# Optimization experiments

Hardware: AMD Instinct MI355X
Metric: run time of the kernel (lower is better)

## Reference

```python
import jax, jax.numpy as jnp
import numpy as np

B, T, D, K = 8, 2048, 384, 64

def setup_inputs() -> dict:
    key = jax.random.key(0)
    k1, k2, k3, k4 = jax.random.split(key, 4)
    x = jax.random.normal(k1, (B, T, D), dtype=jnp.float32)
    # torch nn.Linear default init scale ~ 1/sqrt(fan_in); use scaled normals
    Wq = jax.random.normal(k2, (D, K), dtype=jnp.float32) / np.sqrt(D)
    Wk = jax.random.normal(k3, (D, K), dtype=jnp.float32) / np.sqrt(D)
    Wv = jax.random.normal(k4, (D, D), dtype=jnp.float32) / np.sqrt(D)
    return {"x": x, "Wq": Wq, "Wk": Wk, "Wv": Wv}

def reference(x, Wq, Wk, Wv):
    # x: (B,T,D)
    q = jnp.einsum('btd,dk->btk', x, Wq)      # (B,T,K)
    k = jnp.einsum('btd,dk->btk', x, Wk)      # (B,T,K)
    v = jnp.einsum('btd,de->bte', x, Wv)      # (B,T,D)
    scores = jnp.einsum('bqk,bsk->bqs', q, k) / jnp.sqrt(jnp.float32(K))  # (B,T,T)
    causal = jnp.tril(jnp.ones((T, T), dtype=bool))
    scores = jnp.where(causal, scores, -jnp.inf)
    weights = jax.nn.softmax(scores, axis=-1)
    out = jnp.einsum('bqs,bse->bqe', weights, v)  # (B,T,D)
    return out
```

## Files before the change

### kernel.cpp

```cpp
#include <hip/hip_runtime.h>

#define TT 2048
#define DD 384

typedef float f32x4 __attribute__((ext_vector_type(4)));
typedef float f32x16 __attribute__((ext_vector_type(16)));
typedef short s16x8 __attribute__((ext_vector_type(8)));
typedef short s16x2 __attribute__((ext_vector_type(2)));
typedef unsigned int u32x4 __attribute__((ext_vector_type(4)));

typedef __attribute__((address_space(3))) unsigned char* as3p;
typedef const __attribute__((address_space(1))) unsigned char* as1p;
#define GLLDS(gsrc, ldst) __builtin_amdgcn_global_load_lds((as1p)(gsrc), (as3p)(ldst), 16, 0, 0)

static __device__ __forceinline__ unsigned short f2bf(float f) {
    unsigned int u = __builtin_bit_cast(unsigned int, f);
    u = (u + 0x7fffu + ((u >> 16) & 1u)) >> 16;
    return (unsigned short)u;
}
static __device__ __forceinline__ unsigned int pk2(float a, float b) {
#if __has_builtin(__builtin_amdgcn_cvt_pk_bf16_f32)
    s16x2 t = __builtin_amdgcn_cvt_pk_bf16_f32(a, b);
    return __builtin_bit_cast(unsigned int, t);
#else
    unsigned int ua = __builtin_bit_cast(unsigned int, a);
    unsigned int ub = __builtin_bit_cast(unsigned int, b);
    ua = (ua + 0x7fffu + ((ua >> 16) & 1u)) >> 16;
    ub = (ub + 0x7fffu + ((ub >> 16) & 1u)) & 0xffff0000u;
    return ua | ub;
#endif
}

__global__ __launch_bounds__(256, 2) void qkv_gemm(
    const float* __restrict__ x, const float* __restrict__ Wq,
    const float* __restrict__ Wk, const float* __restrict__ Wv,
    unsigned short* __restrict__ qo, unsigned short* __restrict__ ko,
    unsigned short* __restrict__ vto)
{
    __shared__ __align__(16) unsigned short lds[16384];
    const int tid = threadIdx.x;
    const int l   = tid & 63;
    const int w   = tid >> 6;
    const int si  = l & 15;
    const int qq  = l >> 4;
    const int m0  = blockIdx.x * 128;
    const int nb  = blockIdx.y;
    const int wr  = w >> 1, wc = w & 1;

    const int bn = tid & 127;
    const int bk = (tid >> 7) * 16;
    const float* wsrc; int ldw;
    if (nb == 0) { wsrc = (bn < 64) ? (Wq + bn) : (Wk + (bn - 64)); ldw = 64; }
    else         { wsrc = Wv + (nb - 1) * 128 + bn;                 ldw = 384; }

    f32x4 acc[4][4];
    #pragma unroll
    for (int rt = 0; rt < 4; ++rt)
        #pragma unroll
        for (int ct = 0; ct < 4; ++ct) acc[rt][ct] = (f32x4){0.f, 0.f, 0.f, 0.f};

    for (int kt = 0; kt < 12; ++kt) {
        const int k0 = kt * 32;
        #pragma unroll
        for (int i = 0; i < 2; ++i) {
            const int u = tid + 256 * i, r = u >> 2, c = u & 3;
            const float* xp = x + (size_t)(m0 + r) * DD + k0 + c * 8;
            f32x4 x0 = *(const f32x4*)xp;
            f32x4 x1 = *(const f32x4*)(xp + 4);
            s16x8 av;
            av[0] = (short)f2bf(x0[0]); av[1] = (short)f2bf(x0[1]);
            av[2] = (short)f2bf(x0[2]); av[3] = (short)f2bf(x0[3]);
            av[4] = (short)f2bf(x1[0]); av[5] = (short)f2bf(x1[1]);
            av[6] = (short)f2bf(x1[2]); av[7] = (short)f2bf(x1[3]);
            *(s16x8*)&lds[r * 32 + ((c ^ (r & 3)) * 8)] = av;
        }
        {
            float t[16];
            #pragma unroll
            for (int j = 0; j < 16; ++j) t[j] = wsrc[(size_t)(k0 + bk + j) * ldw];
            #pragma unroll
            for (int jj = 0; jj < 2; ++jj) {
                s16x8 bv;
                #pragma unroll
                for (int j = 0; j < 8; ++j) bv[j] = (short)f2bf(t[jj * 8 + j]);
                const int ch = (tid >> 7) * 2 + jj;
                *(s16x8*)&lds[4096 + bn * 32 + ((ch ^ (bn & 3)) * 8)] = bv;
            }
        }
        __syncthreads();

        s16x8 af[4], bf[4];
        #pragma unroll
        for (int rt = 0; rt < 4; ++rt) {
            const int row = wr * 64 + rt * 16 + si;
            af[rt] = *(const s16x8*)&lds[row * 32 + ((qq ^ (row & 3)) * 8)];
        }
        #pragma unroll
        for (int ct = 0; ct < 4; ++ct) {
            const int col = wc * 64 + ct * 16 + si;
            bf[ct] = *(const s16x8*)&lds[4096 + col * 32 + ((qq ^ (col & 3)) * 8)];
        }
        #pragma unroll
        for (int rt = 0; rt < 4; ++rt)
            #pragma unroll
            for (int ct = 0; ct < 4; ++ct)
                acc[rt][ct] = __builtin_amdgcn_mfma_f32_16x16x32_bf16(af[rt], bf[ct], acc[rt][ct], 0, 0, 0);
        __syncthreads();
    }

    if (nb == 0) {
        if (wc == 0) {
            #pragma unroll
            for (int rt = 0; rt < 4; ++rt)
                #pragma unroll
                for (int ct = 0; ct < 4; ++ct)
                    #pragma unroll
                    for (int r = 0; r < 4; ++r) {
                        const int m = m0 + wr * 64 + rt * 16 + qq * 4 + r;
                        qo[(size_t)m * 64 + ct * 16 + si] = f2bf(acc[rt][ct][r] * 0.125f);
                    }
        } else {
            #pragma unroll
            for (int rt = 0; rt < 4; ++rt)
                #pragma unroll
                for (int ct = 0; ct < 4; ++ct)
                    #pragma unroll
                    for (int r = 0; r < 4; ++r) {
                        const int m = m0 + wr * 64 + rt * 16 + qq * 4 + r;
                        const int col = ct * 16 + si;
                        ko[(size_t)m * 64 + (((col >> 3) ^ (m & 7)) * 8) + (col & 7)] = f2bf(acc[rt][ct][r]);
                    }
        }
    } else {
        #pragma unroll
        for (int rt = 0; rt < 4; ++rt)
            #pragma unroll
            for (int ct = 0; ct < 4; ++ct)
                #pragma unroll
                for (int r = 0; r < 4; ++r) {
                    const int m = wr * 64 + rt * 16 + qq * 4 + r;
                    const int n = wc * 64 + ct * 16 + si;
                    lds[n * 128 + (((m >> 3) ^ (n & 7)) * 8) + (m & 7)] = f2bf(acc[rt][ct][r]);
                }
        __syncthreads();
        const int bbat = m0 >> 11, t0 = m0 & 2047;
        #pragma unroll
        for (int i = 0; i < 8; ++i) {
            const int u = tid + 256 * i, n = u >> 4, mc = u & 15;
            s16x8 v = *(const s16x8*)&lds[n * 128 + ((mc ^ (n & 7)) * 8)];
            *(s16x8*)&vto[((size_t)bbat * DD + ((nb - 1) * 128 + n)) * TT
                          + t0 + (mc >> 3) * 64 + (((mc & 7) ^ (n & 7)) * 8)] = v;
        }
    }
}

__global__ __launch_bounds__(256, 2) void attn(
    const unsigned short* __restrict__ qg, const unsigned short* __restrict__ kg,
    const unsigned short* __restrict__ vg, float* __restrict__ out)
{
    __shared__ __align__(16) unsigned short lds[40960];

    const int tid = threadIdx.x;
    const int l   = tid & 63;
    const int w   = tid >> 6;
    const int qh  = w >> 1;
    const int eg  = w & 1;
    const int lo  = l & 31;
    const int hi  = l >> 5;

    const int g    = blockIdx.x;
    const int bb   = g & 7;
    const int rest = g >> 3;
    const int eh   = rest % 3;
    const int q2   = 31 - rest / 3;
    const int q0   = q2 * 64;
    const int e0   = eh * 128;
    const int qrow = q0 + qh * 32 + lo;

    s16x8 qf[4];
    {
        const unsigned short* qp = qg + ((size_t)bb * TT + qrow) * 64;
        #pragma unroll
        for (int st = 0; st < 4; ++st) qf[st] = *(const s16x8*)(qp + st * 16 + hi * 8);
    }

    f32x16 o[2];
    #pragma unroll
    for (int et = 0; et < 2; ++et)
        #pragma unroll
        for (int r = 0; r < 16; ++r) o[et][r] = 0.f;
    float lp = 0.f;

    const unsigned short* kbase = kg + (size_t)bb * TT * 64;
    const unsigned short* vbase = vg + ((size_t)bb * DD + e0) * TT;

    #define STAGE(IT, KB, VB)                                                              \
    {                                                                                      \
        GLLDS(kbase + (size_t)(IT) * 4096 + (2 * w) * 512 + l * 8,                         \
              &lds[(KB) * 4096 + (2 * w) * 512]);                                          \
        GLLDS(kbase + (size_t)(IT) * 4096 + (2 * w + 1) * 512 + l * 8,                     \
              &lds[(KB) * 4096 + (2 * w + 1) * 512]);                                      \
        _Pragma("unroll")                                                                  \
        for (int c3 = 0; c3 < 4; ++c3) {                                                   \
            const int rg = 4 * w + c3;                                                     \
            GLLDS(vbase + (size_t)(rg * 8 + (l >> 3)) * TT + (IT) * 64 + (l & 7) * 8,      \
                  &lds[8192 + (VB) * 8192 + rg * 512]);                                    \
        }                                                                                  \
    }

    #define PVSTEP(VB, PB)                                                                 \
    {                                                                                      \
        _Pragma("unroll")                                                                  \
        for (int ss = 0; ss < 2; ++ss) {                                                   \
            s16x8 a0 = *(const s16x8*)&lds[32768 + (PB) * 4096 + (qh * 2 + ss) * 1024 + l * 8];       \
            s16x8 a1 = *(const s16x8*)&lds[32768 + (PB) * 4096 + (qh * 2 + ss) * 1024 + 512 + l * 8]; \
            _Pragma("unroll")                                                              \
            for (int et = 0; et < 2; ++et) {                                               \
                const int el = eg * 64 + et * 32 + lo;                                     \
                const int vbse = 8192 + (VB) * 8192 + el * 64;                             \
                s16x8 v0 = *(const s16x8*)&lds[vbse + (((ss * 4 + hi) ^ (el & 7)) * 8)];   \
                o[et] = __builtin_amdgcn_mfma_f32_32x32x16_bf16(a0, v0, o[et], 0, 0, 0);   \
                s16x8 v1 = *(const s16x8*)&lds[vbse + (((ss * 4 + 2 + hi) ^ (el & 7)) * 8)]; \
                o[et] = __builtin_amdgcn_mfma_f32_32x32x16_bf16(a1, v1, o[et], 0, 0, 0);   \
            }                                                                              \
        }                                                                                  \
    }

    STAGE(0, 0, 0);

    int vi = 0, vn = 1;
    for (int it = 0; it <= q2; ++it) {
        const int kb = it & 1;
        __syncthreads();

        if (it < q2) STAGE(it + 1, 1 - kb, vn);

        {
            f32x16 sa;
            #pragma unroll
            for (int r = 0; r < 16; ++r) sa[r] = 0.f;
            #pragma unroll
            for (int st = 0; st < 4; ++st) {
                s16x8 kf = *(const s16x8*)&lds[kb * 4096 + (eg * 32 + lo) * 64 + (((st * 2 + hi) ^ (lo & 7)) * 8)];
                sa = __builtin_amdgcn_mfma_f32_32x32x16_bf16(kf, qf[st], sa, 0, 0, 0);
            }
            const bool mb = (it == q2);
            float pv[16];
            #pragma unroll
            for (int r = 0; r < 16; ++r) {
                float e = __expf(sa[r]);
                if (mb) {
                    const int srow = it * 64 + eg * 32 + (r & 3) + 8 * (r >> 2) + 4 * hi;
                    if (srow > qrow) e = 0.f;
                }
                pv[r] = e;
                lp += e;
            }
            unsigned int d0 = pk2(pv[0], pv[1]),   d1 = pk2(pv[2], pv[3]);
            unsigned int d2 = pk2(pv[4], pv[5]),   d3 = pk2(pv[6], pv[7]);
            unsigned int d4 = pk2(pv[8], pv[9]),   d5 = pk2(pv[10], pv[11]);
            unsigned int d6 = pk2(pv[12], pv[13]), d7 = pk2(pv[14], pv[15]);
            unsigned int sA0 = hi ? d0 : d2, sA1 = hi ? d1 : d3;
            unsigned int rA0 = (unsigned int)__shfl_xor((int)sA0, 32);
            unsigned int rA1 = (unsigned int)__shfl_xor((int)sA1, 32);
            u32x4 fa0 = hi ? (u32x4){rA0, rA1, d2, d3} : (u32x4){d0, d1, rA0, rA1};
            unsigned int sB0 = hi ? d4 : d6, sB1 = hi ? d5 : d7;
            unsigned int rB0 = (unsigned int)__shfl_xor((int)sB0, 32);
            unsigned int rB1 = (unsigned int)__shfl_xor((int)sB1, 32);
            u32x4 fa1 = hi ? (u32x4){rB0, rB1, d6, d7} : (u32x4){d4, d5, rB0, rB1};
            *(s16x8*)&lds[32768 + kb * 4096 + (qh * 2 + eg) * 1024 + l * 8]       = __builtin_bit_cast(s16x8, fa0);
            *(s16x8*)&lds[32768 + kb * 4096 + (qh * 2 + eg) * 1024 + 512 + l * 8] = __builtin_bit_cast(s16x8, fa1);
        }

        if (it > 0) {
            const int vp = (vi == 0) ? 2 : vi - 1;
            PVSTEP(vp, 1 - kb);
        }

        vi = vn; vn = (vn == 2) ? 0 : vn + 1;
    }
    __syncthreads();
    {
        const int vlast = (vi == 0) ? 2 : vi - 1;
        PVSTEP(vlast, q2 & 1);
    }
    __syncthreads();

    float* stL = (float*)&lds[32768];
    lp += __shfl_xor(lp, 32);
    if (hi == 0) stL[(qh * 2 + eg) * 32 + lo] = lp;
    __syncthreads();

    #pragma unroll
    for (int et = 0; et < 2; ++et)
        #pragma unroll
        for (int r = 0; r < 16; ++r) {
            const int rloc = (r & 3) + 8 * (r >> 2) + 4 * hi;
            const float linv = 1.f / (stL[qh * 64 + rloc] + stL[qh * 64 + 32 + rloc]);
            out[((size_t)bb * TT + q0 + qh * 32 + rloc) * DD + e0 + eg * 64 + et * 32 + lo]
                = o[et][r] * linv;
        }
    #undef STAGE
    #undef PVSTEP
}

extern "C" void kernel_launch(void* const* d_in, const int* in_sizes, int n_in,
                              void* d_out, int out_size, void* d_ws, size_t ws_size,
                              hipStream_t stream)
{
    const float* x  = (const float*)d_in[0];
    const float* Wq = (const float*)d_in[1];
    const float* Wk = (const float*)d_in[2];
    const float* Wv = (const float*)d_in[3];

    unsigned short* qws  = (unsigned short*)d_ws;
    unsigned short* kws  = (unsigned short*)((char*)d_ws + ((size_t)2 << 20));
    unsigned short* vtws = (unsigned short*)((char*)d_ws + ((size_t)4 << 20));

    qkv_gemm<<<dim3(128, 4), dim3(256), 0, stream>>>(x, Wq, Wk, Wv, qws, kws, vtws);
    attn<<<dim3(768), dim3(256), 0, stream>>>(qws, kws, vtws, (float*)d_out);
}
```

Before: 140.3 us.

## Pre-convert inputs to bf16, double-buffer QKV GEMM, warp-specialize attention

A new pre-pass kernel converts x and the concatenated weights to swizzled bf16 buffers in workspace. The QKV GEMM then streams them with direct global-to-LDS loads into double-buffered LDS, replacing the in-loop fp32 loads and conversions. The attention kernel is split into producer waves, which compute QK^T and softmax numerators for both query halves, and consumer waves, which run the PV MFMAs, so the two phases overlap. The extra launch and the bf16 round trip through global memory add traffic, and the consumer waves hold twice as many accumulators, raising register pressure.

```diff
diff --git a/kernel.cpp b/kernel.cpp
--- a/kernel.cpp
+++ b/kernel.cpp
@@ -31,9 +31,51 @@
 #endif
 }
 
-__global__ __launch_bounds__(256, 2) void qkv_gemm(
+__global__ __launch_bounds__(256, 8) void xwprep(
     const float* __restrict__ x, const float* __restrict__ Wq,
     const float* __restrict__ Wk, const float* __restrict__ Wv,
+    unsigned short* __restrict__ xbf, unsigned short* __restrict__ wall)
+{
+    const int gid = blockIdx.x * 256 + threadIdx.x;
+    if (gid < 196608) {
+        const int kt = gid >> 14;
+        const int m  = gid & 16383;
+        const float* xp = x + (size_t)m * 384 + kt * 32;
+        unsigned short* op = xbf + (size_t)m * 384 + kt * 32;
+        #pragma unroll
+        for (int c = 0; c < 4; ++c) {
+            f32x4 a = *(const f32x4*)(xp + c * 8);
+            f32x4 b = *(const f32x4*)(xp + c * 8 + 4);
+            s16x8 v;
+            v[0] = (short)f2bf(a[0]); v[1] = (short)f2bf(a[1]);
+            v[2] = (short)f2bf(a[2]); v[3] = (short)f2bf(a[3]);
+            v[4] = (short)f2bf(b[0]); v[5] = (short)f2bf(b[1]);
+            v[6] = (short)f2bf(b[2]); v[7] = (short)f2bf(b[3]);
+            *(s16x8*)(op + ((c ^ (m & 3)) * 8)) = v;
+        }
+    } else {
+        const int gid2 = gid - 196608;
+        const int col = gid2 & 511;
+        const int kt  = gid2 >> 9;
+        unsigned short* op = wall + (size_t)col * 384 + kt * 32;
+        #pragma unroll
+        for (int c = 0; c < 4; ++c) {
+            s16x8 v;
+            #pragma unroll
+            for (int k7 = 0; k7 < 8; ++k7) {
+                const int k = kt * 32 + c * 8 + k7;
+                float f = (col < 64)  ? Wq[(size_t)k * 64 + col]
+                        : (col < 128) ? Wk[(size_t)k * 64 + (col - 64)]
+                                      : Wv[(size_t)k * 384 + (col - 128)];
+                v[k7] = (short)f2bf(f);
+            }
+            *(s16x8*)(op + ((c ^ (col & 3)) * 8)) = v;
+        }
+    }
+}
+
+__global__ __launch_bounds__(256, 4) void qkv_gemm(
+    const unsigned short* __restrict__ xbf, const unsigned short* __restrict__ wall,
     unsigned short* __restrict__ qo, unsigned short* __restrict__ ko,
     unsigned short* __restrict__ vto)
 {
@@ -47,11 +89,18 @@
     const int nb  = blockIdx.y;
     const int wr  = w >> 1, wc = w & 1;
 
-    const int bn = tid & 127;
-    const int bk = (tid >> 7) * 16;
-    const float* wsrc; int ldw;
-    if (nb == 0) { wsrc = (bn < 64) ? (Wq + bn) : (Wk + (bn - 64)); ldw = 64; }
-    else         { wsrc = Wv + (nb - 1) * 128 + bn;                 ldw = 384; }
+    const unsigned short* asrc = xbf + ((size_t)m0 + (l >> 2)) * 384 + (l & 3) * 8;
+    const unsigned short* bsrc = wall + ((size_t)(nb * 128) + (l >> 2)) * 384 + (l & 3) * 8;
+
+#define QSTAGE(KT, B)                                                                     \
+    {                                                                                     \
+        _Pragma("unroll")                                                                 \
+        for (int i = 0; i < 2; ++i) {                                                     \
+            const int u = w * 2 + i;                                                      \
+            GLLDS(asrc + (size_t)(u * 16) * 384 + (KT) * 32, &lds[(B) * 8192 + u * 512]); \
+            GLLDS(bsrc + (size_t)(u * 16) * 384 + (KT) * 32, &lds[(B) * 8192 + 4096 + u * 512]); \
+        }                                                                                 \
+    }
 
     f32x4 acc[4][4];
     #pragma unroll
@@ -59,54 +108,31 @@
         #pragma unroll
         for (int ct = 0; ct < 4; ++ct) acc[rt][ct] = (f32x4){0.f, 0.f, 0.f, 0.f};
 
+    QSTAGE(0, 0);
     for (int kt = 0; kt < 12; ++kt) {
-        const int k0 = kt * 32;
-        #pragma unroll
-        for (int i = 0; i < 2; ++i) {
-            const int u = tid + 256 * i, r = u >> 2, c = u & 3;
-            const float* xp = x + (size_t)(m0 + r) * DD + k0 + c * 8;
-            f32x4 x0 = *(const f32x4*)xp;
-            f32x4 x1 = *(const f32x4*)(xp + 4);
-            s16x8 av;
-            av[0] = (short)f2bf(x0[0]); av[1] = (short)f2bf(x0[1]);
-            av[2] = (short)f2bf(x0[2]); av[3] = (short)f2bf(x0[3]);
-            av[4] = (short)f2bf(x1[0]); av[5] = (short)f2bf(x1[1]);
-            av[6] = (short)f2bf(x1[2]); av[7] = (short)f2bf(x1[3]);
-            *(s16x8*)&lds[r * 32 + ((c ^ (r & 3)) * 8)] = av;
-        }
-        {
-            float t[16];
-            #pragma unroll
-            for (int j = 0; j < 16; ++j) t[j] = wsrc[(size_t)(k0 + bk + j) * ldw];
-            #pragma unroll
-            for (int jj = 0; jj < 2; ++jj) {
-                s16x8 bv;
-                #pragma unroll
-                for (int j = 0; j < 8; ++j) bv[j] = (short)f2bf(t[jj * 8 + j]);
-                const int ch = (tid >> 7) * 2 + jj;
-                *(s16x8*)&lds[4096 + bn * 32 + ((ch ^ (bn & 3)) * 8)] = bv;
-            }
-        }
+        const int b = kt & 1;
         __syncthreads();
+        if (kt < 11) QSTAGE(kt + 1, 1 - b);
 
         s16x8 af[4], bf[4];
         #pragma unroll
         for (int rt = 0; rt < 4; ++rt) {
             const int row = wr * 64 + rt * 16 + si;
-            af[rt] = *(const s16x8*)&lds[row * 32 + ((qq ^ (row & 3)) * 8)];
+            af[rt] = *(const s16x8*)&lds[b * 8192 + row * 32 + ((qq ^ (row & 3)) * 8)];
         }
         #pragma unroll
         for (int ct = 0; ct < 4; ++ct) {
             const int col = wc * 64 + ct * 16 + si;
-            bf[ct] = *(const s16x8*)&lds[4096 + col * 32 + ((qq ^ (col & 3)) * 8)];
+            bf[ct] = *(const s16x8*)&lds[b * 8192 + 4096 + col * 32 + ((qq ^ (col & 3)) * 8)];
         }
         #pragma unroll
         for (int rt = 0; rt < 4; ++rt)
             #pragma unroll
             for (int ct = 0; ct < 4; ++ct)
                 acc[rt][ct] = __builtin_amdgcn_mfma_f32_16x16x32_bf16(af[rt], bf[ct], acc[rt][ct], 0, 0, 0);
-        __syncthreads();
-    }
+    }
+    __syncthreads();
+#undef QSTAGE
 
     if (nb == 0) {
         if (wc == 0) {
@@ -163,8 +189,8 @@
     const int tid = threadIdx.x;
     const int l   = tid & 63;
     const int w   = tid >> 6;
-    const int qh  = w >> 1;
-    const int eg  = w & 1;
+    const int ri  = w & 1;
+    const int prod = (w < 2);
     const int lo  = l & 31;
     const int hi  = l >> 5;
 
@@ -175,53 +201,67 @@
     const int q2   = 31 - rest / 3;
     const int q0   = q2 * 64;
     const int e0   = eh * 128;
-    const int qrow = q0 + qh * 32 + lo;
-
-    s16x8 qf[4];
-    {
-        const unsigned short* qp = qg + ((size_t)bb * TT + qrow) * 64;
-        #pragma unroll
-        for (int st = 0; st < 4; ++st) qf[st] = *(const s16x8*)(qp + st * 16 + hi * 8);
-    }
-
-    f32x16 o[2];
+
+    s16x8 qf2[2][4];
+    if (prod) {
+        #pragma unroll
+        for (int qh = 0; qh < 2; ++qh) {
+            const unsigned short* qp = qg + ((size_t)bb * TT + q0 + qh * 32 + lo) * 64;
+            #pragma unroll
+            for (int st = 0; st < 4; ++st) qf2[qh][st] = *(const s16x8*)(qp + st * 16 + hi * 8);
+        }
+    }
+
+    f32x16 o4[2][2];
     #pragma unroll
-    for (int et = 0; et < 2; ++et)
-        #pragma unroll
-        for (int r = 0; r < 16; ++r) o[et][r] = 0.f;
-    float lp = 0.f;
+    for (int qh = 0; qh < 2; ++qh)
+        #pragma unroll
+        for (int et = 0; et < 2; ++et)
+            #pragma unroll
+            for (int r = 0; r < 16; ++r) o4[qh][et][r] = 0.f;
+    float lp2[2] = {0.f, 0.f};
 
     const unsigned short* kbase = kg + (size_t)bb * TT * 64;
     const unsigned short* vbase = vg + ((size_t)bb * DD + e0) * TT;
 
-    #define STAGE(IT, KB, VB)                                                              \
+#define STAGE(IT, KB, VB)                                                                  \
     {                                                                                      \
-        GLLDS(kbase + (size_t)(IT) * 4096 + (2 * w) * 512 + l * 8,                         \
-              &lds[(KB) * 4096 + (2 * w) * 512]);                                          \
-        GLLDS(kbase + (size_t)(IT) * 4096 + (2 * w + 1) * 512 + l * 8,                     \
-              &lds[(KB) * 4096 + (2 * w + 1) * 512]);                                      \
-        _Pragma("unroll")                                                                  \
-        for (int c3 = 0; c3 < 4; ++c3) {                                                   \
-            const int rg = 4 * w + c3;                                                     \
-            GLLDS(vbase + (size_t)(rg * 8 + (l >> 3)) * TT + (IT) * 64 + (l & 7) * 8,      \
-                  &lds[8192 + (VB) * 8192 + rg * 512]);                                    \
+        if (prod) {                                                                        \
+            _Pragma("unroll")                                                              \
+            for (int c4 = 0; c4 < 4; ++c4) {                                               \
+                const int ch = w * 4 + c4;                                                 \
+                GLLDS(kbase + (size_t)(IT) * 4096 + ch * 512 + l * 8,                      \
+                      &lds[(KB) * 4096 + ch * 512]);                                       \
+            }                                                                              \
+        } else {                                                                           \
+            _Pragma("unroll")                                                              \
+            for (int c8 = 0; c8 < 8; ++c8) {                                               \
+                const int rg = ri * 8 + c8;                                                \
+                GLLDS(vbase + (size_t)(rg * 8 + (l >> 3)) * TT + (IT) * 64 + (l & 7) * 8,  \
+                      &lds[8192 + (VB) * 8192 + rg * 512]);                                \
+            }                                                                              \
         }                                                                                  \
     }
 
-    #define PVSTEP(VB, PB)                                                                 \
+#define PVC(VB, PB)                                                                        \
     {                                                                                      \
         _Pragma("unroll")                                                                  \
-        for (int ss = 0; ss < 2; ++ss) {                                                   \
-            s16x8 a0 = *(const s16x8*)&lds[32768 + (PB) * 4096 + (qh * 2 + ss) * 1024 + l * 8];       \
-            s16x8 a1 = *(const s16x8*)&lds[32768 + (PB) * 4096 + (qh * 2 + ss) * 1024 + 512 + l * 8]; \
+        for (int s2 = 0; s2 < 2; ++s2) {                                                   \
+            const int pbse = 32768 + (PB) * 4096 + s2 * 1024;                              \
+            s16x8 a00 = *(const s16x8*)&lds[pbse + l * 8];                                 \
+            s16x8 a01 = *(const s16x8*)&lds[pbse + 512 + l * 8];                           \
+            s16x8 a10 = *(const s16x8*)&lds[pbse + 2048 + l * 8];                          \
+            s16x8 a11 = *(const s16x8*)&lds[pbse + 2560 + l * 8];                          \
             _Pragma("unroll")                                                              \
             for (int et = 0; et < 2; ++et) {                                               \
-                const int el = eg * 64 + et * 32 + lo;                                     \
+                const int el = ri * 64 + et * 32 + lo;                                     \
                 const int vbse = 8192 + (VB) * 8192 + el * 64;                             \
-                s16x8 v0 = *(const s16x8*)&lds[vbse + (((ss * 4 + hi) ^ (el & 7)) * 8)];   \
-                o[et] = __builtin_amdgcn_mfma_f32_32x32x16_bf16(a0, v0, o[et], 0, 0, 0);   \
-                s16x8 v1 = *(const s16x8*)&lds[vbse + (((ss * 4 + 2 + hi) ^ (el & 7)) * 8)]; \
-                o[et] = __builtin_amdgcn_mfma_f32_32x32x16_bf16(a1, v1, o[et], 0, 0, 0);   \
+                s16x8 v0 = *(const s16x8*)&lds[vbse + (((s2 * 4 + hi) ^ (el & 7)) * 8)];   \
+                s16x8 v1 = *(const s16x8*)&lds[vbse + (((s2 * 4 + 2 + hi) ^ (el & 7)) * 8)]; \
+                o4[0][et] = __builtin_amdgcn_mfma_f32_32x32x16_bf16(a00, v0, o4[0][et], 0, 0, 0); \
+                o4[0][et] = __builtin_amdgcn_mfma_f32_32x32x16_bf16(a01, v1, o4[0][et], 0, 0, 0); \
+                o4[1][et] = __builtin_amdgcn_mfma_f32_32x32x16_bf16(a10, v0, o4[1][et], 0, 0, 0); \
+                o4[1][et] = __builtin_amdgcn_mfma_f32_32x32x16_bf16(a11, v1, o4[1][et], 0, 0, 0); \
             }                                                                              \
         }                                                                                  \
     }
@@ -235,73 +275,84 @@
 
         if (it < q2) STAGE(it + 1, 1 - kb, vn);
 
-        {
-            f32x16 sa;
-            #pragma unroll
-            for (int r = 0; r < 16; ++r) sa[r] = 0.f;
-            #pragma unroll
-            for (int st = 0; st < 4; ++st) {
-                s16x8 kf = *(const s16x8*)&lds[kb * 4096 + (eg * 32 + lo) * 64 + (((st * 2 + hi) ^ (lo & 7)) * 8)];
-                sa = __builtin_amdgcn_mfma_f32_32x32x16_bf16(kf, qf[st], sa, 0, 0, 0);
+        if (prod) {
+            const bool mb = (it == q2);
+            s16x8 kfr[4];
+            #pragma unroll
+            for (int st = 0; st < 4; ++st)
+                kfr[st] = *(const s16x8*)&lds[kb * 4096 + (ri * 32 + lo) * 64 + (((st * 2 + hi) ^ (lo & 7)) * 8)];
+            #pragma unroll
+            for (int qh = 0; qh < 2; ++qh) {
+                const int qrow = q0 + qh * 32 + lo;
+                f32x16 sa;
+                #pragma unroll
+                for (int r = 0; r < 16; ++r) sa[r] = 0.f;
+                #pragma unroll
+                for (int st = 0; st < 4; ++st)
+                    sa = __builtin_amdgcn_mfma_f32_32x32x16_bf16(kfr[st], qf2[qh][st], sa, 0, 0, 0);
+                float pv[16];
+                #pragma unroll
+                for (int r = 0; r < 16; ++r) {
+                    float e = __expf(sa[r]);
+                    if (mb) {
+                        const int srow = it * 64 + ri * 32 + (r & 3) + 8 * (r >> 2) + 4 * hi;
+                        if (srow > qrow) e = 0.f;
+                    }
+                    pv[r] = e;
+                    lp2[qh] += e;
+                }
+                unsigned int d0 = pk2(pv[0], pv[1]),   d1 = pk2(pv[2], pv[3]);
+                unsigned int d2 = pk2(pv[4], pv[5]),   d3 = pk2(pv[6], pv[7]);
+                unsigned int d4 = pk2(pv[8], pv[9]),   d5 = pk2(pv[10], pv[11]);
+                unsigned int d6 = pk2(pv[12], pv[13]), d7 = pk2(pv[14], pv[15]);
+                unsigned int sA0 = hi ? d0 : d2, sA1 = hi ? d1 : d3;
+                unsigned int rA0 = (unsigned int)__shfl_xor((int)sA0, 32);
+                unsigned int rA1 = (unsigned int)__shfl_xor((int)sA1, 32);
+                u32x4 fa0 = hi ? (u32x4){rA0, rA1, d2, d3} : (u32x4){d0, d1, rA0, rA1};
+                unsigned int sB0 = hi ? d4 : d6, sB1 = hi ? d5 : d7;
+                unsigned int rB0 = (unsigned int)__shfl_xor((int)sB0, 32);
+                unsigned int rB1 = (unsigned int)__shfl_xor((int)sB1, 32);
+                u32x4 fa1 = hi ? (u32x4){rB0, rB1, d6, d7} : (u32x4){d4, d5, rB0, rB1};
+                *(s16x8*)&lds[32768 + kb * 4096 + (qh * 2 + ri) * 1024 + l * 8]       = __builtin_bit_cast(s16x8, fa0);
+                *(s16x8*)&lds[32768 + kb * 4096 + (qh * 2 + ri) * 1024 + 512 + l * 8] = __builtin_bit_cast(s16x8, fa1);
             }
-            const bool mb = (it == q2);
-            float pv[16];
-            #pragma unroll
-            for (int r = 0; r < 16; ++r) {
-                float e = __expf(sa[r]);
-                if (mb) {
-                    const int srow = it * 64 + eg * 32 + (r & 3) + 8 * (r >> 2) + 4 * hi;
-                    if (srow > qrow) e = 0.f;
+        } else if (it > 0) {
+            const int vp = (vi == 0) ? 2 : vi - 1;
+            PVC(vp, 1 - kb);
+        }
+
+        vi = vn; vn = (vn == 2) ? 0 : vn + 1;
+    }
+    __syncthreads();
+
+    if (prod) {
+        #pragma unroll
+        for (int qh = 0; qh < 2; ++qh) {
+            float lp = lp2[qh] + __shfl_xor(lp2[qh], 32);
+            if (hi == 0) ((float*)lds)[(qh * 2 + ri) * 32 + lo] = lp;
+        }
+    } else {
+        const int vlast = (vi == 0) ? 2 : vi - 1;
+        PVC(vlast, q2 & 1);
+    }
+    __syncthreads();
+
+    if (!prod) {
+        const float* stL = (const float*)lds;
+        #pragma unroll
+        for (int qh = 0; qh < 2; ++qh)
+            #pragma unroll
+            for (int et = 0; et < 2; ++et)
+                #pragma unroll
+                for (int r = 0; r < 16; ++r) {
+                    const int rloc = (r & 3) + 8 * (r >> 2) + 4 * hi;
+                    const float linv = 1.f / (stL[qh * 64 + rloc] + stL[qh * 64 + 32 + rloc]);
+                    out[((size_t)bb * TT + q0 + qh * 32 + rloc) * DD + e0 + ri * 64 + et * 32 + lo]
+                        = o4[qh][et][r] * linv;
                 }
-                pv[r] = e;
-                lp += e;
-            }
-            unsigned int d0 = pk2(pv[0], pv[1]),   d1 = pk2(pv[2], pv[3]);
-            unsigned int d2 = pk2(pv[4], pv[5]),   d3 = pk2(pv[6], pv[7]);
-            unsigned int d4 = pk2(pv[8], pv[9]),   d5 = pk2(pv[10], pv[11]);
-            unsigned int d6 = pk2(pv[12], pv[13]), d7 = pk2(pv[14], pv[15]);
-            unsigned int sA0 = hi ? d0 : d2, sA1 = hi ? d1 : d3;
-            unsigned int rA0 = (unsigned int)__shfl_xor((int)sA0, 32);
-            unsigned int rA1 = (unsigned int)__shfl_xor((int)sA1, 32);
-            u32x4 fa0 = hi ? (u32x4){rA0, rA1, d2, d3} : (u32x4){d0, d1, rA0, rA1};
-            unsigned int sB0 = hi ? d4 : d6, sB1 = hi ? d5 : d7;
-            unsigned int rB0 = (unsigned int)__shfl_xor((int)sB0, 32);
-            unsigned int rB1 = (unsigned int)__shfl_xor((int)sB1, 32);
-            u32x4 fa1 = hi ? (u32x4){rB0, rB1, d6, d7} : (u32x4){d4, d5, rB0, rB1};
-            *(s16x8*)&lds[32768 + kb * 4096 + (qh * 2 + eg) * 1024 + l * 8]       = __builtin_bit_cast(s16x8, fa0);
-            *(s16x8*)&lds[32768 + kb * 4096 + (qh * 2 + eg) * 1024 + 512 + l * 8] = __builtin_bit_cast(s16x8, fa1);
-        }
-
-        if (it > 0) {
-            const int vp = (vi == 0) ? 2 : vi - 1;
-            PVSTEP(vp, 1 - kb);
-        }
-
-        vi = vn; vn = (vn == 2) ? 0 : vn + 1;
-    }
-    __syncthreads();
-    {
-        const int vlast = (vi == 0) ? 2 : vi - 1;
-        PVSTEP(vlast, q2 & 1);
-    }
-    __syncthreads();
-
-    float* stL = (float*)&lds[32768];
-    lp += __shfl_xor(lp, 32);
-    if (hi == 0) stL[(qh * 2 + eg) * 32 + lo] = lp;
-    __syncthreads();
-
-    #pragma unroll
-    for (int et = 0; et < 2; ++et)
-        #pragma unroll
-        for (int r = 0; r < 16; ++r) {
-            const int rloc = (r & 3) + 8 * (r >> 2) + 4 * hi;
-            const float linv = 1.f / (stL[qh * 64 + rloc] + stL[qh * 64 + 32 + rloc]);
-            out[((size_t)bb * TT + q0 + qh * 32 + rloc) * DD + e0 + eg * 64 + et * 32 + lo]
-                = o[et][r] * linv;
-        }
-    #undef STAGE
-    #undef PVSTEP
+    }
+#undef STAGE
+#undef PVC
 }
 
 extern "C" void kernel_launch(void* const* d_in, const int* in_sizes, int n_in,
@@ -316,7 +367,10 @@
     unsigned short* qws  = (unsigned short*)d_ws;
     unsigned short* kws  = (unsigned short*)((char*)d_ws + ((size_t)2 << 20));
     unsigned short* vtws = (unsigned short*)((char*)d_ws + ((size_t)4 << 20));
-
-    qkv_gemm<<<dim3(128, 4), dim3(256), 0, stream>>>(x, Wq, Wk, Wv, qws, kws, vtws);
+    unsigned short* xbf  = (unsigned short*)((char*)d_ws + ((size_t)16 << 20));
+    unsigned short* wall = (unsigned short*)((char*)d_ws + ((size_t)28 << 20));
+
+    xwprep<<<dim3(792), dim3(256), 0, stream>>>(x, Wq, Wk, Wv, xbf, wall);
+    qkv_gemm<<<dim3(128, 4), dim3(256), 0, stream>>>(xbf, wall, qws, kws, vtws);
     attn<<<dim3(768), dim3(256), 0, stream>>>(qws, kws, vtws, (float*)d_out);
 }
```

After: 152.1 us. 8.4% more time.
